# Kernel optimization log

Measured on AMD Instinct MI355X. Metric: run time of the kernel, lower is better.

The kernel has to match this reference:

```python
import jax, jax.numpy as jnp
import numpy as np

# MACE/molgym-style SimpleModel with max_ell=1, hidden_irreps = 64x0e + 64x1o,
# num_interactions=2, num_elements=10, num_bessel=8, polynomial cutoff p=5, r_max=5.0.
N, E, C, NE, NB, H = 20000, 320000, 64, 10, 8, 64
R_MAX = 5.0
P_CUT = 5


def _mlp(x, W1, W2, W3):
    # radial MLP producing per-edge tensor-product weights (silu nonlinearity)
    h = jax.nn.silu(x @ W1)
    h = jax.nn.silu(h @ W2)
    return h @ W3


def setup_inputs() -> dict:
    key = jax.random.key(0)
    ks = jax.random.split(key, 24)
    positions = jax.random.normal(ks[0], (N, 3), jnp.float32)
    edge_index = jax.random.randint(ks[1], (2, E), 0, N)
    shifts = jnp.zeros((E, 3), jnp.float32)
    species = jax.random.randint(ks[2], (N,), 0, NE)
    node_attrs = jax.nn.one_hot(species, NE, dtype=jnp.float32)

    def w(k, shape, fan_in):
        return jax.random.normal(k, shape, jnp.float32) / np.sqrt(fan_in)

    params = dict(
        W_embed=w(ks[3], (NE, C), NE),
        R1_W1=w(ks[4], (NB, H), NB), R1_W2=w(ks[5], (H, H), H), R1_W3=w(ks[6], (H, 2 * C), H),
        U1_s=w(ks[7], (C, C), C),
        L1_s=w(ks[8], (C, C), C), L1_v=w(ks[9], (C, C), C),
        K1_s=w(ks[10], (C, NE, C), C * NE),
        R2_W1=w(ks[11], (NB, H), NB), R2_W2=w(ks[12], (H, H), H), R2_W3=w(ks[13], (H, 4 * C), H),
        U2_s=w(ks[14], (C, C), C), U2_v=w(ks[15], (C, C), C),
        L2_s=w(ks[16], (2 * C, C), 2 * C), L2_v=w(ks[17], (2 * C, C), 2 * C),
        K2_s=w(ks[18], (C, NE, C), C * NE), K2_v=w(ks[19], (C, NE, C), C * NE),
    )
    return dict(positions=positions, node_attrs=node_attrs, edge_index=edge_index,
                shifts=shifts, **params)


def _forward(positions, node_attrs, shifts, W_embed,
             R1_W1, R1_W2, R1_W3, U1_s, L1_s, L1_v, K1_s,
             R2_W1, R2_W2, R2_W3, U2_s, U2_v, L2_s, L2_v, K2_s, K2_v,
             edge_index):
    snd, rcv = edge_index[0], edge_index[1]
    # edge vectors / lengths
    vec = positions[snd] - positions[rcv] + shifts            # [E,3]
    length = jnp.sqrt(jnp.sum(vec * vec, axis=1, keepdims=True) + 1e-12)  # [E,1]
    unit = vec / length
    # spherical harmonics (normalize=True, component normalization): Y0=1, Y1=sqrt(3)*r_hat
    Y1 = np.float32(np.sqrt(3.0)) * unit                      # [E,3]
    # Bessel radial basis * polynomial cutoff
    n = jnp.arange(1, NB + 1, dtype=jnp.float32)
    bessel = np.float32(np.sqrt(2.0 / R_MAX)) * jnp.sin(n * np.float32(np.pi) * length / R_MAX) / length
    u = length / R_MAX
    p = P_CUT
    poly = (1.0 - 0.5 * (p + 1) * (p + 2) * u ** p
            + p * (p + 2) * u ** (p + 1)
            - 0.5 * p * (p + 1) * u ** (p + 2))
    edge_feats = bessel * (poly * (u < 1.0))                  # [E,NB]
    # node embedding (linear on one-hot species)
    s0 = node_attrs @ W_embed                                 # [N,C]

    # ---- interaction block 1 (input feats: scalars only) ----
    s = s0 @ U1_s                                             # linear_up
    tpw = _mlp(edge_feats, R1_W1, R1_W2, R1_W3).reshape(E, 2, C)
    s_e = s[snd]                                              # gather sender feats
    m_s = tpw[:, 0] * s_e                                     # 0e x 0e -> 0e  [E,C]
    m_v = (tpw[:, 1] * s_e)[:, :, None] * Y1[:, None, :]      # 0e x 1o -> 1o  [E,C,3]
    agg_s = jax.ops.segment_sum(m_s, rcv, num_segments=N)
    agg_v = jax.ops.segment_sum(m_v, rcv, num_segments=N)
    skip_s = jnp.einsum('nu,nv,uvd->nd', s0, node_attrs, K1_s)  # skip tensor product
    s1 = agg_s @ L1_s + skip_s                                # [N,C]
    v1 = jnp.einsum('nci,cd->ndi', agg_v, L1_v)               # [N,C,3]

    # ---- interaction block 2 (input feats: 64x0e + 64x1o) ----
    s = s1 @ U2_s
    v = jnp.einsum('nci,cd->ndi', v1, U2_v)
    tpw = _mlp(edge_feats, R2_W1, R2_W2, R2_W3).reshape(E, 4, C)
    s_e, v_e = s[snd], v[snd]
    mA = tpw[:, 0] * s_e                                      # 0e x 0e -> 0e
    mB = (tpw[:, 1] * s_e)[:, :, None] * Y1[:, None, :]       # 0e x 1o -> 1o
    mC = tpw[:, 2][:, :, None] * v_e                          # 1o x 0e -> 1o
    mD = tpw[:, 3] * (jnp.einsum('eci,ei->ec', v_e, Y1) / np.float32(np.sqrt(3.0)))  # 1o x 1o -> 0e
    mid_s = jnp.concatenate([mA, mD], axis=1)                 # [E,2C]
    mid_v = jnp.concatenate([mB, mC], axis=1)                 # [E,2C,3]
    agg_s = jax.ops.segment_sum(mid_s, rcv, num_segments=N)
    agg_v = jax.ops.segment_sum(mid_v, rcv, num_segments=N)
    skip_s = jnp.einsum('nu,nv,uvd->nd', s1, node_attrs, K2_s)
    skip_v = jnp.einsum('nui,nv,uvd->ndi', v1, node_attrs, K2_v)
    s2 = agg_s @ L2_s + skip_s                                # [N,C]
    v2 = jnp.einsum('nci,cd->ndi', agg_v, L2_v) + skip_v      # [N,C,3]
    return jnp.concatenate([s2, v2.reshape(N, 3 * C)], axis=1)  # [N,4C]


def reference(positions, node_attrs, edge_index, shifts, W_embed,
              R1_W1, R1_W2, R1_W3, U1_s, L1_s, L1_v, K1_s,
              R2_W1, R2_W2, R2_W3, U2_s, U2_v, L2_s, L2_v, K2_s, K2_v):
    return _forward(positions, node_attrs, shifts, W_embed,
                    R1_W1, R1_W2, R1_W3, U1_s, L1_s, L1_v, K1_s,
                    R2_W1, R2_W2, R2_W3, U2_s, U2_v, L2_s, L2_v, K2_s, K2_v,
                    edge_index)
```

## Files before the change

kernel.cpp:

```cpp
#include <hip/hip_runtime.h>

#define NNODES 20000
#define NEDGES 320000
#define NELEM  10
#define NC     (NNODES * 64)

#define OFF_SUP1 ((size_t)0)
#define OFF_AGS1 ((size_t)1 * NC)
#define OFF_AGV1 ((size_t)2 * NC)
#define OFF_AGS2 ((size_t)0)
#define OFF_AGV2 ((size_t)2 * NC)
#define OFF_SUP2 ((size_t)8 * NC)
#define OFF_VUP2 ((size_t)9 * NC)
#define OFF_SKS2 ((size_t)12 * NC)
#define OFF_SKV2 ((size_t)13 * NC)
#define OFF_INT  ((size_t)16 * NC)

#define SMEM_BYTES 52480

typedef __attribute__((ext_vector_type(8))) short bf16x8;
typedef __attribute__((ext_vector_type(4))) float f32x4;

__device__ __forceinline__ float silu(float x) { return x / (1.0f + __expf(-x)); }
__device__ __forceinline__ int rfl(int v) { return __builtin_amdgcn_readfirstlane(v); }
__device__ __forceinline__ int rl_i(int v, int l) { return __builtin_amdgcn_readlane(v, l); }
__device__ __forceinline__ float rl_f(float v, int l) {
    return __int_as_float(__builtin_amdgcn_readlane(__float_as_int(v), l));
}
__device__ __forceinline__ uint2 split2(float x0, float x1) {
    unsigned int b0 = __float_as_uint(x0), b1 = __float_as_uint(x1);
    unsigned int h0 = (b0 + 0x7FFF + ((b0 >> 16) & 1)) & 0xFFFF0000u;
    unsigned int h1 = (b1 + 0x7FFF + ((b1 >> 16) & 1)) & 0xFFFF0000u;
    unsigned int l0 = __float_as_uint(x0 - __uint_as_float(h0));
    unsigned int l1 = __float_as_uint(x1 - __uint_as_float(h1));
    unsigned int hi = (h0 >> 16) | (h1 & 0xFFFF0000u);
    unsigned int lo = ((l0 + 0x7FFF + ((l0 >> 16) & 1)) >> 16)
                    | ((l1 + 0x7FFF + ((l1 >> 16) & 1)) & 0xFFFF0000u);
    return make_uint2(hi, lo);
}

__global__ __launch_bounds__(256) void k_wsplit(
    const float* __restrict__ W3a, const float* __restrict__ W3b,
    unsigned short* __restrict__ out)
{
    int t = blockIdx.x * 256 + threadIdx.x;
    float x; unsigned short *ph, *pl; int idx;
    if (t < 8192) {
        int n = t >> 6, k = t & 63;
        x = W3a[k * 128 + n]; ph = out; pl = out + 8192; idx = n * 64 + k;
    } else {
        int u = t - 8192; int n = u >> 6, k = u & 63;
        x = W3b[k * 256 + n]; ph = out + 16384; pl = out + 32768; idx = n * 64 + k;
    }
    unsigned int b = __float_as_uint(x);
    unsigned int h = (b + 0x7FFF + ((b >> 16) & 1)) & 0xFFFF0000u;
    unsigned int r = __float_as_uint(x - __uint_as_float(h));
    ph[idx] = (unsigned short)(h >> 16);
    pl[idx] = (unsigned short)((r + 0x7FFF + ((r >> 16) & 1)) >> 16);
}

__global__ __launch_bounds__(256) void k_hist(const int* __restrict__ eidx,
                                              int* __restrict__ hist)
{
    int e = blockIdx.x * 256 + threadIdx.x;
    atomicAdd(&hist[eidx[NEDGES + e]], 1);
}

__global__ __launch_bounds__(1024) void k_scan(const int* __restrict__ hist,
                                               int* __restrict__ cursor)
{
    __shared__ int wsum[16];
    __shared__ int gbase;
    int tid = threadIdx.x;
    int lane = tid & 63, wvid = tid >> 6;
    if (tid == 0) gbase = 0;
    __syncthreads();
    for (int seg = 0; seg < 20; ++seg) {
        int i = seg * 1024 + tid;
        int v = (i < NNODES) ? hist[i] : 0;
        int s = v;
        #pragma unroll
        for (int d = 1; d < 64; d <<= 1) {
            int t = __shfl_up(s, d, 64);
            if (lane >= d) s += t;
        }
        if (lane == 63) wsum[wvid] = s;
        __syncthreads();
        if (wvid == 0) {
            int w = (lane < 16) ? wsum[lane] : 0;
            #pragma unroll
            for (int d = 1; d < 16; d <<= 1) {
                int t = __shfl_up(w, d, 64);
                if (lane >= d) w += t;
            }
            if (lane < 16) wsum[lane] = w;
        }
        __syncthreads();
        int wbase = (wvid == 0) ? 0 : wsum[wvid - 1];
        if (i < NNODES) cursor[i] = gbase + wbase + s - v;
        int segtot = wsum[15];
        __syncthreads();
        if (tid == 0) gbase += segtot;
    }
}

__global__ __launch_bounds__(256) void k_scatter(const int* __restrict__ eidx,
                                                 int* __restrict__ cursor,
                                                 int* __restrict__ sorted)
{
    int e = blockIdx.x * 256 + threadIdx.x;
    int pos = atomicAdd(&cursor[eidx[NEDGES + e]], 1);
    sorted[pos] = e;
}

__global__ __launch_bounds__(256) void k_node_pre(
    const float* __restrict__ attrs, const float* __restrict__ Wemb,
    const float* __restrict__ U1s, float* __restrict__ sUp1)
{
    int lane = threadIdx.x & 63, wv = threadIdx.x >> 6;
    int n = blockIdx.x * 4 + wv;
    __shared__ __align__(16) float s0sh[4][64];
    float s0 = 0.f;
    #pragma unroll
    for (int v = 0; v < NELEM; ++v) s0 += attrs[n * NELEM + v] * Wemb[v * 64 + lane];
    s0sh[wv][lane] = s0;
    __syncthreads();
    float a = 0.f;
    #pragma unroll 8
    for (int k = 0; k < 64; ++k) a += s0sh[wv][k] * U1s[k * 64 + lane];
    sUp1[n * 64 + lane] = a;
}

__global__ __launch_bounds__(256, 3) void k_edge1(
    const float* __restrict__ pos, const int* __restrict__ eidx,
    const float* __restrict__ shf, const int* __restrict__ sorted,
    const float* __restrict__ W1, const float* __restrict__ W2,
    const unsigned short* __restrict__ w3h, const unsigned short* __restrict__ w3l,
    const float* __restrict__ sUp1,
    float* __restrict__ agS1, float* __restrict__ agV1)
{
    __shared__ __align__(16) char smem[SMEM_BYTES];
    float (*ysh)[3]   = (float (*)[3])(smem);
    int*  ssh         = (int*)(smem + 768);
    int*  rsh         = (int*)(smem + 1024);
    float (*h1sh)[65] = (float (*)[65])(smem + 1280);
    float (*fsh)[9]   = (float (*)[9])(smem + 17920);
    unsigned short (*h2buf)[64][72] = (unsigned short (*)[64][72])(smem + 34048);

    const int tid = threadIdx.x;
    const int lane = tid & 63;
    const int w = rfl(tid >> 6);
    const int e0 = blockIdx.x * 64;

    {
        int e = tid >> 2, sub = tid & 3;
        int sid = sorted[e0 + e];
        int snd = eidx[sid], rcv = eidx[NEDGES + sid];
        float dx = pos[snd * 3 + 0] - pos[rcv * 3 + 0] + shf[(size_t)sid * 3 + 0];
        float dy = pos[snd * 3 + 1] - pos[rcv * 3 + 1] + shf[(size_t)sid * 3 + 1];
        float dz = pos[snd * 3 + 2] - pos[rcv * 3 + 2] + shf[(size_t)sid * 3 + 2];
        float len = sqrtf(dx * dx + dy * dy + dz * dz + 1e-12f);
        float inv = 1.0f / len;
        float u = len * 0.2f;
        float u2 = u * u, u4 = u2 * u2, u5 = u4 * u, u6 = u5 * u, u7 = u6 * u;
        float cut = (u < 1.0f) ? (1.0f - 21.0f * u5 + 35.0f * u6 - 15.0f * u7) : 0.0f;
        float s = 0.632455532033676f * inv * cut;
        #pragma unroll
        for (int kk = 0; kk < 2; ++kk) {
            int k = sub * 2 + kk;
            fsh[e][k] = s * sinf((float)(k + 1) * 0.628318530717959f * len);
        }
        if (sub == 0) {
            ssh[e] = snd; rsh[e] = rcv;
            ysh[e][0] = 1.73205080756888f * dx * inv;
            ysh[e][1] = 1.73205080756888f * dy * inv;
            ysh[e][2] = 1.73205080756888f * dz * inv;
        }
    }
    __syncthreads();

    const int rAll = rsh[lane];
    const int sAll = ssh[lane];
    const float y0A = ysh[lane][0], y1A = ysh[lane][1], y2A = ysh[lane][2];

    {
        float f[8];
        #pragma unroll
        for (int k = 0; k < 8; ++k) f[k] = fsh[lane][k];
        const float* __restrict__ w1b = W1 + w * 16;
        #pragma unroll
        for (int j = 0; j < 16; ++j) {
            float a = 0.f;
            #pragma unroll
            for (int k = 0; k < 8; ++k) a = fmaf(f[k], w1b[k * 64 + j], a);
            h1sh[lane][w * 16 + j] = silu(a);
        }
    }
    __syncthreads();

    {
        const float2* __restrict__ w2b = (const float2*)W2 + w * 8;
        float2 acc[8];
        #pragma unroll
        for (int j = 0; j < 8; ++j) acc[j] = make_float2(0.f, 0.f);
        for (int k = 0; k < 64; ++k) {
            float h = h1sh[lane][k];
            const float2* __restrict__ wk = w2b + k * 32;
            #pragma unroll
            for (int j = 0; j < 8; ++j) {
                float2 wv = wk[j];
                acc[j].x = fmaf(h, wv.x, acc[j].x);
                acc[j].y = fmaf(h, wv.y, acc[j].y);
            }
        }
        #pragma unroll
        for (int j = 0; j < 8; ++j) {
            uint2 p = split2(silu(acc[j].x), silu(acc[j].y));
            *(unsigned int*)&h2buf[0][lane][w * 16 + 2 * j] = p.x;
            *(unsigned int*)&h2buf[1][lane][w * 16 + 2 * j] = p.y;
        }
    }
    __syncthreads();

    const int q = lane >> 4, nl = lane & 15;
    float* trw = (float*)(smem + 1280) + w * 2048;

    const unsigned short* ar = &h2buf[0][w * 16 + nl][0];
    const unsigned short* al = &h2buf[1][w * 16 + nl][0];
    bf16x8 ah0 = *(const bf16x8*)(ar + q * 8);
    bf16x8 ah1 = *(const bf16x8*)(ar + 32 + q * 8);
    bf16x8 al0 = *(const bf16x8*)(al + q * 8);
    bf16x8 al1 = *(const bf16x8*)(al + 32 + q * 8);

    float sreg[16];
    #pragma unroll
    for (int i = 0; i < 16; ++i)
        sreg[i] = sUp1[rl_i(sAll, w * 16 + i) * 64 + lane];

    #pragma unroll
    for (int nt = 0; nt < 8; ++nt) {
        int ng = nt * 16 + nl;
        const unsigned short* wh = w3h + ng * 64 + q * 8;
        const unsigned short* wl = w3l + ng * 64 + q * 8;
        bf16x8 bh0 = *(const bf16x8*)wh;
        bf16x8 bh1 = *(const bf16x8*)(wh + 32);
        bf16x8 bl0 = *(const bf16x8*)wl;
        bf16x8 bl1 = *(const bf16x8*)(wl + 32);
        f32x4 a = {0.f, 0.f, 0.f, 0.f};
        a = __builtin_amdgcn_mfma_f32_16x16x32_bf16(ah0, bh0, a, 0, 0, 0);
        a = __builtin_amdgcn_mfma_f32_16x16x32_bf16(ah1, bh1, a, 0, 0, 0);
        a = __builtin_amdgcn_mfma_f32_16x16x32_bf16(ah0, bl0, a, 0, 0, 0);
        a = __builtin_amdgcn_mfma_f32_16x16x32_bf16(ah1, bl1, a, 0, 0, 0);
        a = __builtin_amdgcn_mfma_f32_16x16x32_bf16(al0, bh0, a, 0, 0, 0);
        a = __builtin_amdgcn_mfma_f32_16x16x32_bf16(al1, bh1, a, 0, 0, 0);
        #pragma unroll
        for (int r = 0; r < 4; ++r) {
            int li = q * 4 + r;
            trw[li * 128 + ((ng + 4 * li) & 127)] = a[r];
        }
    }

    float accS = 0.f, b0 = 0.f, b1 = 0.f, b2 = 0.f;
    int cur = rl_i(rAll, w * 16);
    #pragma unroll
    for (int i = 0; i < 16; ++i) {
        int e = w * 16 + i;
        int rcv = rl_i(rAll, e);
        if (rcv != cur) {
            unsafeAtomicAdd(&agS1[cur * 64 + lane], accS);
            unsafeAtomicAdd(&agV1[cur * 192 +       lane], b0);
            unsafeAtomicAdd(&agV1[cur * 192 +  64 + lane], b1);
            unsafeAtomicAdd(&agV1[cur * 192 + 128 + lane], b2);
            accS = b0 = b1 = b2 = 0.f;
            cur = rcv;
        }
        float tv0 = trw[i * 128 + ((lane + 4 * i) & 127)];
        float tv1 = trw[i * 128 + ((64 + lane + 4 * i) & 127)];
        float se = sreg[i];
        accS += tv0 * se;
        float msg = tv1 * se;
        b0 += msg * rl_f(y0A, e);
        b1 += msg * rl_f(y1A, e);
        b2 += msg * rl_f(y2A, e);
    }
    unsafeAtomicAdd(&agS1[cur * 64 + lane], accS);
    unsafeAtomicAdd(&agV1[cur * 192 +       lane], b0);
    unsafeAtomicAdd(&agV1[cur * 192 +  64 + lane], b1);
    unsafeAtomicAdd(&agV1[cur * 192 + 128 + lane], b2);
}

__global__ __launch_bounds__(256) void k_node_mid(
    const float* __restrict__ attrs, const float* __restrict__ Wemb,
    const float* __restrict__ K1s, const float* __restrict__ L1s,
    const float* __restrict__ L1v,
    const float* __restrict__ U2s, const float* __restrict__ U2v,
    const float* __restrict__ K2s, const float* __restrict__ K2v,
    const float* __restrict__ agS1, const float* __restrict__ agV1,
    float* __restrict__ sUp2, float* __restrict__ vUp2,
    float* __restrict__ skS2, float* __restrict__ skV2)
{
    int lane = threadIdx.x & 63, wv = threadIdx.x >> 6;
    int n = blockIdx.x * 4 + wv;
    __shared__ float aSsh[4][64];
    __shared__ float aVsh[4][3][64];
    __shared__ float s0sh[4][64];
    __shared__ float s1sh[4][64];
    __shared__ float v1sh[4][3][64];

    int sp = 0;
    #pragma unroll
    for (int v = 0; v < NELEM; ++v) if (attrs[n * NELEM + v] > 0.5f) sp = v;
    aSsh[wv][lane] = agS1[n * 64 + lane];
    #pragma unroll
    for (int i = 0; i < 3; ++i) aVsh[wv][i][lane] = agV1[n * 192 + i * 64 + lane];
    s0sh[wv][lane] = Wemb[sp * 64 + lane];
    __syncthreads();

    float s1 = 0.f;
    #pragma unroll 8
    for (int k = 0; k < 64; ++k) s1 += aSsh[wv][k] * L1s[k * 64 + lane];
    #pragma unroll 8
    for (int k = 0; k < 64; ++k) s1 += s0sh[wv][k] * K1s[(k * NELEM + sp) * 64 + lane];
    float v1[3] = {0.f, 0.f, 0.f};
    #pragma unroll 8
    for (int k = 0; k < 64; ++k) {
        float w = L1v[k * 64 + lane];
        v1[0] += aVsh[wv][0][k] * w;
        v1[1] += aVsh[wv][1][k] * w;
        v1[2] += aVsh[wv][2][k] * w;
    }
    s1sh[wv][lane] = s1;
    #pragma unroll
    for (int i = 0; i < 3; ++i) v1sh[wv][i][lane] = v1[i];
    __syncthreads();

    float su = 0.f, ks = 0.f;
    float vu[3] = {0.f, 0.f, 0.f}, kv[3] = {0.f, 0.f, 0.f};
    #pragma unroll 8
    for (int k = 0; k < 64; ++k) su += s1sh[wv][k] * U2s[k * 64 + lane];
    #pragma unroll 8
    for (int k = 0; k < 64; ++k) ks += s1sh[wv][k] * K2s[(k * NELEM + sp) * 64 + lane];
    #pragma unroll 8
    for (int k = 0; k < 64; ++k) {
        float w = U2v[k * 64 + lane];
        vu[0] += v1sh[wv][0][k] * w;
        vu[1] += v1sh[wv][1][k] * w;
        vu[2] += v1sh[wv][2][k] * w;
    }
    #pragma unroll 8
    for (int k = 0; k < 64; ++k) {
        float w = K2v[(k * NELEM + sp) * 64 + lane];
        kv[0] += v1sh[wv][0][k] * w;
        kv[1] += v1sh[wv][1][k] * w;
        kv[2] += v1sh[wv][2][k] * w;
    }
    sUp2[n * 64 + lane] = su;
    skS2[n * 64 + lane] = ks;
    #pragma unroll
    for (int i = 0; i < 3; ++i) {
        vUp2[n * 192 + i * 64 + lane] = vu[i];
        skV2[n * 192 + i * 64 + lane] = kv[i];
    }
}

__global__ __launch_bounds__(256, 3) void k_edge2(
    const float* __restrict__ pos, const int* __restrict__ eidx,
    const float* __restrict__ shf, const int* __restrict__ sorted,
    const float* __restrict__ W1, const float* __restrict__ W2,
    const unsigned short* __restrict__ w3h, const unsigned short* __restrict__ w3l,
    const float* __restrict__ sUp2, const float* __restrict__ vUp2,
    float* __restrict__ agS2, float* __restrict__ agV2)
{
    __shared__ __align__(16) char smem[SMEM_BYTES];
    float (*ysh)[3]   = (float (*)[3])(smem);
    int*  ssh         = (int*)(smem + 768);
    int*  rsh         = (int*)(smem + 1024);
    float (*h1sh)[65] = (float (*)[65])(smem + 1280);
    float (*fsh)[9]   = (float (*)[9])(smem + 17920);
    unsigned short (*h2buf)[64][72] = (unsigned short (*)[64][72])(smem + 34048);

    const int tid = threadIdx.x;
    const int lane = tid & 63;
    const int w = rfl(tid >> 6);
    const int e0 = blockIdx.x * 64;

    {
        int e = tid >> 2, sub = tid & 3;
        int sid = sorted[e0 + e];
        int snd = eidx[sid], rcv = eidx[NEDGES + sid];
        float dx = pos[snd * 3 + 0] - pos[rcv * 3 + 0] + shf[(size_t)sid * 3 + 0];
        float dy = pos[snd * 3 + 1] - pos[rcv * 3 + 1] + shf[(size_t)sid * 3 + 1];
        float dz = pos[snd * 3 + 2] - pos[rcv * 3 + 2] + shf[(size_t)sid * 3 + 2];
        float len = sqrtf(dx * dx + dy * dy + dz * dz + 1e-12f);
        float inv = 1.0f / len;
        float u = len * 0.2f;
        float u2 = u * u, u4 = u2 * u2, u5 = u4 * u, u6 = u5 * u, u7 = u6 * u;
        float cut = (u < 1.0f) ? (1.0f - 21.0f * u5 + 35.0f * u6 - 15.0f * u7) : 0.0f;
        float s = 0.632455532033676f * inv * cut;
        #pragma unroll
        for (int kk = 0; kk < 2; ++kk) {
            int k = sub * 2 + kk;
            fsh[e][k] = s * sinf((float)(k + 1) * 0.628318530717959f * len);
        }
        if (sub == 0) {
            ssh[e] = snd; rsh[e] = rcv;
            ysh[e][0] = 1.73205080756888f * dx * inv;
            ysh[e][1] = 1.73205080756888f * dy * inv;
            ysh[e][2] = 1.73205080756888f * dz * inv;
        }
    }
    __syncthreads();

    const int rAll = rsh[lane];
    const int sAll = ssh[lane];
    const float y0A = ysh[lane][0], y1A = ysh[lane][1], y2A = ysh[lane][2];

    {
        float f[8];
        #pragma unroll
        for (int k = 0; k < 8; ++k) f[k] = fsh[lane][k];
        const float* __restrict__ w1b = W1 + w * 16;
        #pragma unroll
        for (int j = 0; j < 16; ++j) {
            float a = 0.f;
            #pragma unroll
            for (int k = 0; k < 8; ++k) a = fmaf(f[k], w1b[k * 64 + j], a);
            h1sh[lane][w * 16 + j] = silu(a);
        }
    }
    __syncthreads();

    {
        const float2* __restrict__ w2b = (const float2*)W2 + w * 8;
        float2 acc[8];
        #pragma unroll
        for (int j = 0; j < 8; ++j) acc[j] = make_float2(0.f, 0.f);
        for (int k = 0; k < 64; ++k) {
            float h = h1sh[lane][k];
            const float2* __restrict__ wk = w2b + k * 32;
            #pragma unroll
            for (int j = 0; j < 8; ++j) {
                float2 wv = wk[j];
                acc[j].x = fmaf(h, wv.x, acc[j].x);
                acc[j].y = fmaf(h, wv.y, acc[j].y);
            }
        }
        #pragma unroll
        for (int j = 0; j < 8; ++j) {
            uint2 p = split2(silu(acc[j].x), silu(acc[j].y));
            *(unsigned int*)&h2buf[0][lane][w * 16 + 2 * j] = p.x;
            *(unsigned int*)&h2buf[1][lane][w * 16 + 2 * j] = p.y;
        }
    }
    __syncthreads();

    const int q = lane >> 4, nl = lane & 15;
    float* trw = (float*)(smem + 1280) + w * 2048;

    const unsigned short* ar = &h2buf[0][w * 16 + nl][0];
    const unsigned short* al = &h2buf[1][w * 16 + nl][0];
    bf16x8 ah0 = *(const bf16x8*)(ar + q * 8);
    bf16x8 ah1 = *(const bf16x8*)(ar + 32 + q * 8);
    bf16x8 al0 = *(const bf16x8*)(al + q * 8);
    bf16x8 al1 = *(const bf16x8*)(al + 32 + q * 8);

    float sreg[16];
    #pragma unroll
    for (int i = 0; i < 16; ++i)
        sreg[i] = sUp2[rl_i(sAll, w * 16 + i) * 64 + lane];

    #pragma unroll
    for (int nt = 0; nt < 8; ++nt) {
        int ng = nt * 16 + nl;
        const unsigned short* wh = w3h + ng * 64 + q * 8;
        const unsigned short* wl = w3l + ng * 64 + q * 8;
        bf16x8 bh0 = *(const bf16x8*)wh;
        bf16x8 bh1 = *(const bf16x8*)(wh + 32);
        bf16x8 bl0 = *(const bf16x8*)wl;
        bf16x8 bl1 = *(const bf16x8*)(wl + 32);
        f32x4 a = {0.f, 0.f, 0.f, 0.f};
        a = __builtin_amdgcn_mfma_f32_16x16x32_bf16(ah0, bh0, a, 0, 0, 0);
        a = __builtin_amdgcn_mfma_f32_16x16x32_bf16(ah1, bh1, a, 0, 0, 0);
        a = __builtin_amdgcn_mfma_f32_16x16x32_bf16(ah0, bl0, a, 0, 0, 0);
        a = __builtin_amdgcn_mfma_f32_16x16x32_bf16(ah1, bl1, a, 0, 0, 0);
        a = __builtin_amdgcn_mfma_f32_16x16x32_bf16(al0, bh0, a, 0, 0, 0);
        a = __builtin_amdgcn_mfma_f32_16x16x32_bf16(al1, bh1, a, 0, 0, 0);
        #pragma unroll
        for (int r = 0; r < 4; ++r) {
            int li = q * 4 + r;
            trw[li * 128 + ((ng + 4 * li) & 127)] = a[r];
        }
    }

    {
        float accS = 0.f, b0 = 0.f, b1 = 0.f, b2 = 0.f;
        int cur = rl_i(rAll, w * 16);
        #pragma unroll
        for (int i = 0; i < 16; ++i) {
            int e = w * 16 + i;
            int rcv = rl_i(rAll, e);
            if (rcv != cur) {
                unsafeAtomicAdd(&agS2[cur * 128 + lane], accS);
                unsafeAtomicAdd(&agV2[cur * 384 + 0 * 128 + lane], b0);
                unsafeAtomicAdd(&agV2[cur * 384 + 1 * 128 + lane], b1);
                unsafeAtomicAdd(&agV2[cur * 384 + 2 * 128 + lane], b2);
                accS = b0 = b1 = b2 = 0.f;
                cur = rcv;
            }
            float tv0 = trw[i * 128 + ((lane + 4 * i) & 127)];
            float tv1 = trw[i * 128 + ((64 + lane + 4 * i) & 127)];
            float se = sreg[i];
            accS += tv0 * se;
            float msg = tv1 * se;
            b0 += msg * rl_f(y0A, e);
            b1 += msg * rl_f(y1A, e);
            b2 += msg * rl_f(y2A, e);
        }
        unsafeAtomicAdd(&agS2[cur * 128 + lane], accS);
        unsafeAtomicAdd(&agV2[cur * 384 + 0 * 128 + lane], b0);
        unsafeAtomicAdd(&agV2[cur * 384 + 1 * 128 + lane], b1);
        unsafeAtomicAdd(&agV2[cur * 384 + 2 * 128 + lane], b2);
    }

    float vr0[16], vr1[16], vr2[16];
    #pragma unroll
    for (int i = 0; i < 16; ++i) {
        int snd = rl_i(sAll, w * 16 + i);
        vr0[i] = vUp2[snd * 192 +       lane];
        vr1[i] = vUp2[snd * 192 +  64 + lane];
        vr2[i] = vUp2[snd * 192 + 128 + lane];
    }

    #pragma unroll
    for (int nt = 0; nt < 8; ++nt) {
        int c  = nt * 16 + nl;
        int ng = 128 + c;
        const unsigned short* wh = w3h + ng * 64 + q * 8;
        const unsigned short* wl = w3l + ng * 64 + q * 8;
        bf16x8 bh0 = *(const bf16x8*)wh;
        bf16x8 bh1 = *(const bf16x8*)(wh + 32);
        bf16x8 bl0 = *(const bf16x8*)wl;
        bf16x8 bl1 = *(const bf16x8*)(wl + 32);
        f32x4 a = {0.f, 0.f, 0.f, 0.f};
        a = __builtin_amdgcn_mfma_f32_16x16x32_bf16(ah0, bh0, a, 0, 0, 0);
        a = __builtin_amdgcn_mfma_f32_16x16x32_bf16(ah1, bh1, a, 0, 0, 0);
        a = __builtin_amdgcn_mfma_f32_16x16x32_bf16(ah0, bl0, a, 0, 0, 0);
        a = __builtin_amdgcn_mfma_f32_16x16x32_bf16(ah1, bl1, a, 0, 0, 0);
        a = __builtin_amdgcn_mfma_f32_16x16x32_bf16(al0, bh0, a, 0, 0, 0);
        a = __builtin_amdgcn_mfma_f32_16x16x32_bf16(al1, bh1, a, 0, 0, 0);
        #pragma unroll
        for (int r = 0; r < 4; ++r) {
            int li = q * 4 + r;
            trw[li * 128 + ((c + 4 * li) & 127)] = a[r];
        }
    }

    {
        float accD = 0.f, c0 = 0.f, c1 = 0.f, c2 = 0.f;
        int cur = rl_i(rAll, w * 16);
        #pragma unroll
        for (int i = 0; i < 16; ++i) {
            int e = w * 16 + i;
            int rcv = rl_i(rAll, e);
            if (rcv != cur) {
                unsafeAtomicAdd(&agS2[cur * 128 + 64 + lane], accD);
                unsafeAtomicAdd(&agV2[cur * 384 + 0 * 128 + 64 + lane], c0);
                unsafeAtomicAdd(&agV2[cur * 384 + 1 * 128 + 64 + lane], c1);
                unsafeAtomicAdd(&agV2[cur * 384 + 2 * 128 + 64 + lane], c2);
                accD = c0 = c1 = c2 = 0.f;
                cur = rcv;
            }
            float tvC = trw[i * 128 + ((lane + 4 * i) & 127)];
            float tvD = trw[i * 128 + ((64 + lane + 4 * i) & 127)];
            c0 += tvC * vr0[i];
            c1 += tvC * vr1[i];
            c2 += tvC * vr2[i];
            float dotvy = vr0[i] * rl_f(y0A, e) + vr1[i] * rl_f(y1A, e)
                        + vr2[i] * rl_f(y2A, e);
            accD += tvD * dotvy * 0.577350269189626f;
        }
        unsafeAtomicAdd(&agS2[cur * 128 + 64 + lane], accD);
        unsafeAtomicAdd(&agV2[cur * 384 + 0 * 128 + 64 + lane], c0);
        unsafeAtomicAdd(&agV2[cur * 384 + 1 * 128 + 64 + lane], c1);
        unsafeAtomicAdd(&agV2[cur * 384 + 2 * 128 + 64 + lane], c2);
    }
}

__global__ __launch_bounds__(256) void k_node_out(
    const float* __restrict__ L2s, const float* __restrict__ L2v,
    const float* __restrict__ agS2, const float* __restrict__ agV2,
    const float* __restrict__ skS2, const float* __restrict__ skV2,
    float* __restrict__ out)
{
    int lane = threadIdx.x & 63, wv = threadIdx.x >> 6;
    int n = blockIdx.x * 4 + wv;
    __shared__ __align__(16) float aS[4][128];
    __shared__ __align__(16) float aV[4][3][128];

    aS[wv][lane]      = agS2[n * 128 + lane];
    aS[wv][64 + lane] = agS2[n * 128 + 64 + lane];
    #pragma unroll
    for (int i = 0; i < 3; ++i) {
        aV[wv][i][lane]      = agV2[n * 384 + i * 128 + lane];
        aV[wv][i][64 + lane] = agV2[n * 384 + i * 128 + 64 + lane];
    }
    __syncthreads();

    float s2 = skS2[n * 64 + lane];
    #pragma unroll 8
    for (int u = 0; u < 128; ++u) s2 += aS[wv][u] * L2s[u * 64 + lane];
    float v2[3];
    #pragma unroll
    for (int i = 0; i < 3; ++i) v2[i] = skV2[n * 192 + i * 64 + lane];
    #pragma unroll 8
    for (int u = 0; u < 128; ++u) {
        float w = L2v[u * 64 + lane];
        v2[0] += aV[wv][0][u] * w;
        v2[1] += aV[wv][1][u] * w;
        v2[2] += aV[wv][2][u] * w;
    }
    out[(size_t)n * 256 + lane] = s2;
    #pragma unroll
    for (int i = 0; i < 3; ++i)
        out[(size_t)n * 256 + 64 + lane * 3 + i] = v2[i];
}

extern "C" void kernel_launch(void* const* d_in, const int* in_sizes, int n_in,
                              void* d_out, int out_size, void* d_ws, size_t ws_size,
                              hipStream_t stream)
{
    (void)in_sizes; (void)n_in; (void)out_size; (void)ws_size;
    const float* positions  = (const float*)d_in[0];
    const float* node_attrs = (const float*)d_in[1];
    const int*   edge_index = (const int*)d_in[2];
    const float* shifts     = (const float*)d_in[3];
    const float* W_embed    = (const float*)d_in[4];
    const float* R1W1 = (const float*)d_in[5];
    const float* R1W2 = (const float*)d_in[6];
    const float* R1W3 = (const float*)d_in[7];
    const float* U1s  = (const float*)d_in[8];
    const float* L1s  = (const float*)d_in[9];
    const float* L1v  = (const float*)d_in[10];
    const float* K1s  = (const float*)d_in[11];
    const float* R2W1 = (const float*)d_in[12];
    const float* R2W2 = (const float*)d_in[13];
    const float* R2W3 = (const float*)d_in[14];
    const float* U2s  = (const float*)d_in[15];
    const float* U2v  = (const float*)d_in[16];
    const float* L2s  = (const float*)d_in[17];
    const float* L2v  = (const float*)d_in[18];
    const float* K2s  = (const float*)d_in[19];
    const float* K2v  = (const float*)d_in[20];

    float* wsf = (float*)d_ws;
    int*   wsi = (int*)(wsf + OFF_INT);
    int* hist   = wsi;
    int* cursor = wsi + 20000;
    int* sorted = wsi + 40000;
    unsigned short* wsh = (unsigned short*)(wsi + 360000);
    const unsigned short* w3a_hi = wsh;
    const unsigned short* w3a_lo = wsh + 8192;
    const unsigned short* w3b_hi = wsh + 16384;
    const unsigned short* w3b_lo = wsh + 32768;

    hipMemsetAsync(wsf + OFF_AGS1, 0, (size_t)4 * NC * sizeof(float), stream);
    hipMemsetAsync(hist, 0, 20000 * sizeof(int), stream);

    k_wsplit<<<96, 256, 0, stream>>>(R1W3, R2W3, wsh);
    k_hist<<<NEDGES / 256, 256, 0, stream>>>(edge_index, hist);
    k_scan<<<1, 1024, 0, stream>>>(hist, cursor);
    k_scatter<<<NEDGES / 256, 256, 0, stream>>>(edge_index, cursor, sorted);

    k_node_pre<<<NNODES / 4, 256, 0, stream>>>(node_attrs, W_embed, U1s, wsf + OFF_SUP1);
    k_edge1<<<NEDGES / 64, 256, 0, stream>>>(positions, edge_index, shifts, sorted,
                                             R1W1, R1W2, w3a_hi, w3a_lo,
                                             wsf + OFF_SUP1, wsf + OFF_AGS1, wsf + OFF_AGV1);
    k_node_mid<<<NNODES / 4, 256, 0, stream>>>(node_attrs, W_embed, K1s, L1s, L1v,
                                               U2s, U2v, K2s, K2v,
                                               wsf + OFF_AGS1, wsf + OFF_AGV1,
                                               wsf + OFF_SUP2, wsf + OFF_VUP2,
                                               wsf + OFF_SKS2, wsf + OFF_SKV2);
    hipMemsetAsync(wsf + OFF_AGS2, 0, (size_t)8 * NC * sizeof(float), stream);
    k_edge2<<<NEDGES / 64, 256, 0, stream>>>(positions, edge_index, shifts, sorted,
                                             R2W1, R2W2, w3b_hi, w3b_lo,
                                             wsf + OFF_SUP2, wsf + OFF_VUP2,
                                             wsf + OFF_AGS2, wsf + OFF_AGV2);
    k_node_out<<<NNODES / 4, 256, 0, stream>>>(L2s, L2v, wsf + OFF_AGS2, wsf + OFF_AGV2,
                                               wsf + OFF_SKS2, wsf + OFF_SKV2,
                                               (float*)d_out);
}
```

Measured before the change: 633.1 us.

## Halve per-wave tpw staging buffer to shrink LDS and raise edge-kernel occupancy

```diff
diff --git a/kernel.cpp b/kernel.cpp
--- a/kernel.cpp
+++ b/kernel.cpp
@@ -16,7 +16,7 @@
 #define OFF_SKV2 ((size_t)13 * NC)
 #define OFF_INT  ((size_t)16 * NC)
 
-#define SMEM_BYTES 52480
+#define SMEM_BYTES 38656
 
 typedef __attribute__((ext_vector_type(8))) short bf16x8;
 typedef __attribute__((ext_vector_type(4))) float f32x4;
@@ -131,7 +131,7 @@
     sUp1[n * 64 + lane] = a;
 }
 
-__global__ __launch_bounds__(256, 3) void k_edge1(
+__global__ __launch_bounds__(256, 4) void k_edge1(
     const float* __restrict__ pos, const int* __restrict__ eidx,
     const float* __restrict__ shf, const int* __restrict__ sorted,
     const float* __restrict__ W1, const float* __restrict__ W2,
@@ -144,8 +144,8 @@
     int*  ssh         = (int*)(smem + 768);
     int*  rsh         = (int*)(smem + 1024);
     float (*h1sh)[65] = (float (*)[65])(smem + 1280);
-    float (*fsh)[9]   = (float (*)[9])(smem + 17920);
-    unsigned short (*h2buf)[64][72] = (unsigned short (*)[64][72])(smem + 34048);
+    unsigned short (*h2buf)[64][72] = (unsigned short (*)[64][72])(smem + 17920);
+    float (*fsh)[9]   = (float (*)[9])(smem + 36352);
 
     const int tid = threadIdx.x;
     const int lane = tid & 63;
@@ -223,7 +223,7 @@
     __syncthreads();
 
     const int q = lane >> 4, nl = lane & 15;
-    float* trw = (float*)(smem + 1280) + w * 2048;
+    float* trw = (float*)(smem + 1280) + w * 1024;
 
     const unsigned short* ar = &h2buf[0][w * 16 + nl][0];
     const unsigned short* al = &h2buf[1][w * 16 + nl][0];
@@ -238,8 +238,47 @@
         sreg[i] = sUp1[rl_i(sAll, w * 16 + i) * 64 + lane];
 
     #pragma unroll
-    for (int nt = 0; nt < 8; ++nt) {
-        int ng = nt * 16 + nl;
+    for (int nt = 0; nt < 4; ++nt) {
+        int c = nt * 16 + nl;
+        const unsigned short* wh = w3h + c * 64 + q * 8;
+        const unsigned short* wl = w3l + c * 64 + q * 8;
+        bf16x8 bh0 = *(const bf16x8*)wh;
+        bf16x8 bh1 = *(const bf16x8*)(wh + 32);
+        bf16x8 bl0 = *(const bf16x8*)wl;
+        bf16x8 bl1 = *(const bf16x8*)(wl + 32);
+        f32x4 a = {0.f, 0.f, 0.f, 0.f};
+        a = __builtin_amdgcn_mfma_f32_16x16x32_bf16(ah0, bh0, a, 0, 0, 0);
+        a = __builtin_amdgcn_mfma_f32_16x16x32_bf16(ah1, bh1, a, 0, 0, 0);
+        a = __builtin_amdgcn_mfma_f32_16x16x32_bf16(ah0, bl0, a, 0, 0, 0);
+        a = __builtin_amdgcn_mfma_f32_16x16x32_bf16(ah1, bl1, a, 0, 0, 0);
+        a = __builtin_amdgcn_mfma_f32_16x16x32_bf16(al0, bh0, a, 0, 0, 0);
+        a = __builtin_amdgcn_mfma_f32_16x16x32_bf16(al1, bh1, a, 0, 0, 0);
+        #pragma unroll
+        for (int r = 0; r < 4; ++r) {
+            int li = q * 4 + r;
+            trw[li * 64 + ((c + 4 * li) & 63)] = a[r];
+        }
+    }
+    {
+        float accS = 0.f;
+        int cur = rl_i(rAll, w * 16);
+        #pragma unroll
+        for (int i = 0; i < 16; ++i) {
+            int e = w * 16 + i;
+            int rcv = rl_i(rAll, e);
+            if (rcv != cur) {
+                unsafeAtomicAdd(&agS1[cur * 64 + lane], accS);
+                accS = 0.f; cur = rcv;
+            }
+            accS += trw[i * 64 + ((lane + 4 * i) & 63)] * sreg[i];
+        }
+        unsafeAtomicAdd(&agS1[cur * 64 + lane], accS);
+    }
+
+    #pragma unroll
+    for (int nt = 0; nt < 4; ++nt) {
+        int c = nt * 16 + nl;
+        int ng = 64 + c;
         const unsigned short* wh = w3h + ng * 64 + q * 8;
         const unsigned short* wl = w3l + ng * 64 + q * 8;
         bf16x8 bh0 = *(const bf16x8*)wh;
@@ -256,37 +295,31 @@
         #pragma unroll
         for (int r = 0; r < 4; ++r) {
             int li = q * 4 + r;
-            trw[li * 128 + ((ng + 4 * li) & 127)] = a[r];
-        }
-    }
-
-    float accS = 0.f, b0 = 0.f, b1 = 0.f, b2 = 0.f;
-    int cur = rl_i(rAll, w * 16);
-    #pragma unroll
-    for (int i = 0; i < 16; ++i) {
-        int e = w * 16 + i;
-        int rcv = rl_i(rAll, e);
-        if (rcv != cur) {
-            unsafeAtomicAdd(&agS1[cur * 64 + lane], accS);
-            unsafeAtomicAdd(&agV1[cur * 192 +       lane], b0);
-            unsafeAtomicAdd(&agV1[cur * 192 +  64 + lane], b1);
-            unsafeAtomicAdd(&agV1[cur * 192 + 128 + lane], b2);
-            accS = b0 = b1 = b2 = 0.f;
-            cur = rcv;
-        }
-        float tv0 = trw[i * 128 + ((lane + 4 * i) & 127)];
-        float tv1 = trw[i * 128 + ((64 + lane + 4 * i) & 127)];
-        float se = sreg[i];
-        accS += tv0 * se;
-        float msg = tv1 * se;
-        b0 += msg * rl_f(y0A, e);
-        b1 += msg * rl_f(y1A, e);
-        b2 += msg * rl_f(y2A, e);
-    }
-    unsafeAtomicAdd(&agS1[cur * 64 + lane], accS);
-    unsafeAtomicAdd(&agV1[cur * 192 +       lane], b0);
-    unsafeAtomicAdd(&agV1[cur * 192 +  64 + lane], b1);
-    unsafeAtomicAdd(&agV1[cur * 192 + 128 + lane], b2);
+            trw[li * 64 + ((c + 4 * li) & 63)] = a[r];
+        }
+    }
+    {
+        float b0 = 0.f, b1 = 0.f, b2 = 0.f;
+        int cur = rl_i(rAll, w * 16);
+        #pragma unroll
+        for (int i = 0; i < 16; ++i) {
+            int e = w * 16 + i;
+            int rcv = rl_i(rAll, e);
+            if (rcv != cur) {
+                unsafeAtomicAdd(&agV1[cur * 192 +       lane], b0);
+                unsafeAtomicAdd(&agV1[cur * 192 +  64 + lane], b1);
+                unsafeAtomicAdd(&agV1[cur * 192 + 128 + lane], b2);
+                b0 = b1 = b2 = 0.f; cur = rcv;
+            }
+            float msg = trw[i * 64 + ((lane + 4 * i) & 63)] * sreg[i];
+            b0 += msg * rl_f(y0A, e);
+            b1 += msg * rl_f(y1A, e);
+            b2 += msg * rl_f(y2A, e);
+        }
+        unsafeAtomicAdd(&agV1[cur * 192 +       lane], b0);
+        unsafeAtomicAdd(&agV1[cur * 192 +  64 + lane], b1);
+        unsafeAtomicAdd(&agV1[cur * 192 + 128 + lane], b2);
+    }
 }
 
 __global__ __launch_bounds__(256) void k_node_mid(
@@ -363,7 +396,7 @@
     }
 }
 
-__global__ __launch_bounds__(256, 3) void k_edge2(
+__global__ __launch_bounds__(256, 4) void k_edge2(
     const float* __restrict__ pos, const int* __restrict__ eidx,
     const float* __restrict__ shf, const int* __restrict__ sorted,
     const float* __restrict__ W1, const float* __restrict__ W2,
@@ -376,8 +409,8 @@
     int*  ssh         = (int*)(smem + 768);
     int*  rsh         = (int*)(smem + 1024);
     float (*h1sh)[65] = (float (*)[65])(smem + 1280);
-    float (*fsh)[9]   = (float (*)[9])(smem + 17920);
-    unsigned short (*h2buf)[64][72] = (unsigned short (*)[64][72])(smem + 34048);
+    unsigned short (*h2buf)[64][72] = (unsigned short (*)[64][72])(smem + 17920);
+    float (*fsh)[9]   = (float (*)[9])(smem + 36352);
 
     const int tid = threadIdx.x;
     const int lane = tid & 63;
@@ -455,7 +488,7 @@
     __syncthreads();
 
     const int q = lane >> 4, nl = lane & 15;
-    float* trw = (float*)(smem + 1280) + w * 2048;
+    float* trw = (float*)(smem + 1280) + w * 1024;
 
     const unsigned short* ar = &h2buf[0][w * 16 + nl][0];
     const unsigned short* al = &h2buf[1][w * 16 + nl][0];
@@ -470,8 +503,47 @@
         sreg[i] = sUp2[rl_i(sAll, w * 16 + i) * 64 + lane];
 
     #pragma unroll
-    for (int nt = 0; nt < 8; ++nt) {
-        int ng = nt * 16 + nl;
+    for (int nt = 0; nt < 4; ++nt) {
+        int c = nt * 16 + nl;
+        const unsigned short* wh = w3h + c * 64 + q * 8;
+        const unsigned short* wl = w3l + c * 64 + q * 8;
+        bf16x8 bh0 = *(const bf16x8*)wh;
+        bf16x8 bh1 = *(const bf16x8*)(wh + 32);
+        bf16x8 bl0 = *(const bf16x8*)wl;
+        bf16x8 bl1 = *(const bf16x8*)(wl + 32);
+        f32x4 a = {0.f, 0.f, 0.f, 0.f};
+        a = __builtin_amdgcn_mfma_f32_16x16x32_bf16(ah0, bh0, a, 0, 0, 0);
+        a = __builtin_amdgcn_mfma_f32_16x16x32_bf16(ah1, bh1, a, 0, 0, 0);
+        a = __builtin_amdgcn_mfma_f32_16x16x32_bf16(ah0, bl0, a, 0, 0, 0);
+        a = __builtin_amdgcn_mfma_f32_16x16x32_bf16(ah1, bl1, a, 0, 0, 0);
+        a = __builtin_amdgcn_mfma_f32_16x16x32_bf16(al0, bh0, a, 0, 0, 0);
+        a = __builtin_amdgcn_mfma_f32_16x16x32_bf16(al1, bh1, a, 0, 0, 0);
+        #pragma unroll
+        for (int r = 0; r < 4; ++r) {
+            int li = q * 4 + r;
+            trw[li * 64 + ((c + 4 * li) & 63)] = a[r];
+        }
+    }
+    {
+        float accS = 0.f;
+        int cur = rl_i(rAll, w * 16);
+        #pragma unroll
+        for (int i = 0; i < 16; ++i) {
+            int e = w * 16 + i;
+            int rcv = rl_i(rAll, e);
+            if (rcv != cur) {
+                unsafeAtomicAdd(&agS2[cur * 128 + lane], accS);
+                accS = 0.f; cur = rcv;
+            }
+            accS += trw[i * 64 + ((lane + 4 * i) & 63)] * sreg[i];
+        }
+        unsafeAtomicAdd(&agS2[cur * 128 + lane], accS);
+    }
+
+    #pragma unroll
+    for (int nt = 0; nt < 4; ++nt) {
+        int c = nt * 16 + nl;
+        int ng = 64 + c;
         const unsigned short* wh = w3h + ng * 64 + q * 8;
         const unsigned short* wl = w3l + ng * 64 + q * 8;
         bf16x8 bh0 = *(const bf16x8*)wh;
@@ -488,35 +560,27 @@
         #pragma unroll
         for (int r = 0; r < 4; ++r) {
             int li = q * 4 + r;
-            trw[li * 128 + ((ng + 4 * li) & 127)] = a[r];
-        }
-    }
-
-    {
-        float accS = 0.f, b0 = 0.f, b1 = 0.f, b2 = 0.f;
+            trw[li * 64 + ((c + 4 * li) & 63)] = a[r];
+        }
+    }
+    {
+        float b0 = 0.f, b1 = 0.f, b2 = 0.f;
         int cur = rl_i(rAll, w * 16);
         #pragma unroll
         for (int i = 0; i < 16; ++i) {
             int e = w * 16 + i;
             int rcv = rl_i(rAll, e);
             if (rcv != cur) {
-                unsafeAtomicAdd(&agS2[cur * 128 + lane], accS);
                 unsafeAtomicAdd(&agV2[cur * 384 + 0 * 128 + lane], b0);
                 unsafeAtomicAdd(&agV2[cur * 384 + 1 * 128 + lane], b1);
                 unsafeAtomicAdd(&agV2[cur * 384 + 2 * 128 + lane], b2);
-                accS = b0 = b1 = b2 = 0.f;
-                cur = rcv;
-            }
-            float tv0 = trw[i * 128 + ((lane + 4 * i) & 127)];
-            float tv1 = trw[i * 128 + ((64 + lane + 4 * i) & 127)];
-            float se = sreg[i];
-            accS += tv0 * se;
-            float msg = tv1 * se;
+                b0 = b1 = b2 = 0.f; cur = rcv;
+            }
+            float msg = trw[i * 64 + ((lane + 4 * i) & 63)] * sreg[i];
             b0 += msg * rl_f(y0A, e);
             b1 += msg * rl_f(y1A, e);
             b2 += msg * rl_f(y2A, e);
         }
-        unsafeAtomicAdd(&agS2[cur * 128 + lane], accS);
         unsafeAtomicAdd(&agV2[cur * 384 + 0 * 128 + lane], b0);
         unsafeAtomicAdd(&agV2[cur * 384 + 1 * 128 + lane], b1);
         unsafeAtomicAdd(&agV2[cur * 384 + 2 * 128 + lane], b2);
@@ -532,8 +596,8 @@
     }
 
     #pragma unroll
-    for (int nt = 0; nt < 8; ++nt) {
-        int c  = nt * 16 + nl;
+    for (int nt = 0; nt < 4; ++nt) {
+        int c = nt * 16 + nl;
         int ng = 128 + c;
         const unsigned short* wh = w3h + ng * 64 + q * 8;
         const unsigned short* wl = w3l + ng * 64 + q * 8;
@@ -551,12 +615,57 @@
         #pragma unroll
         for (int r = 0; r < 4; ++r) {
             int li = q * 4 + r;
-            trw[li * 128 + ((c + 4 * li) & 127)] = a[r];
-        }
-    }
-
-    {
-        float accD = 0.f, c0 = 0.f, c1 = 0.f, c2 = 0.f;
+            trw[li * 64 + ((c + 4 * li) & 63)] = a[r];
+        }
+    }
+    {
+        float c0 = 0.f, c1 = 0.f, c2 = 0.f;
+        int cur = rl_i(rAll, w * 16);
+        #pragma unroll
+        for (int i = 0; i < 16; ++i) {
+            int e = w * 16 + i;
+            int rcv = rl_i(rAll, e);
+            if (rcv != cur) {
+                unsafeAtomicAdd(&agV2[cur * 384 + 0 * 128 + 64 + lane], c0);
+                unsafeAtomicAdd(&agV2[cur * 384 + 1 * 128 + 64 + lane], c1);
+                unsafeAtomicAdd(&agV2[cur * 384 + 2 * 128 + 64 + lane], c2);
+                c0 = c1 = c2 = 0.f; cur = rcv;
+            }
+            float tvC = trw[i * 64 + ((lane + 4 * i) & 63)];
+            c0 += tvC * vr0[i];
+            c1 += tvC * vr1[i];
+            c2 += tvC * vr2[i];
+        }
+        unsafeAtomicAdd(&agV2[cur * 384 + 0 * 128 + 64 + lane], c0);
+        unsafeAtomicAdd(&agV2[cur * 384 + 1 * 128 + 64 + lane], c1);
+        unsafeAtomicAdd(&agV2[cur * 384 + 2 * 128 + 64 + lane], c2);
+    }
+
+    #pragma unroll
+    for (int nt = 0; nt < 4; ++nt) {
+        int c = nt * 16 + nl;
+        int ng = 192 + c;
+        const unsigned short* wh = w3h + ng * 64 + q * 8;
+        const unsigned short* wl = w3l + ng * 64 + q * 8;
+        bf16x8 bh0 = *(const bf16x8*)wh;
+        bf16x8 bh1 = *(const bf16x8*)(wh + 32);
+        bf16x8 bl0 = *(const bf16x8*)wl;
+        bf16x8 bl1 = *(const bf16x8*)(wl + 32);
+        f32x4 a = {0.f, 0.f, 0.f, 0.f};
+        a = __builtin_amdgcn_mfma_f32_16x16x32_bf16(ah0, bh0, a, 0, 0, 0);
+        a = __builtin_amdgcn_mfma_f32_16x16x32_bf16(ah1, bh1, a, 0, 0, 0);
+        a = __builtin_amdgcn_mfma_f32_16x16x32_bf16(ah0, bl0, a, 0, 0, 0);
+        a = __builtin_amdgcn_mfma_f32_16x16x32_bf16(ah1, bl1, a, 0, 0, 0);
+        a = __builtin_amdgcn_mfma_f32_16x16x32_bf16(al0, bh0, a, 0, 0, 0);
+        a = __builtin_amdgcn_mfma_f32_16x16x32_bf16(al1, bh1, a, 0, 0, 0);
+        #pragma unroll
+        for (int r = 0; r < 4; ++r) {
+            int li = q * 4 + r;
+            trw[li * 64 + ((c + 4 * li) & 63)] = a[r];
+        }
+    }
+    {
+        float accD = 0.f;
         int cur = rl_i(rAll, w * 16);
         #pragma unroll
         for (int i = 0; i < 16; ++i) {
@@ -564,25 +673,14 @@
             int rcv = rl_i(rAll, e);
             if (rcv != cur) {
                 unsafeAtomicAdd(&agS2[cur * 128 + 64 + lane], accD);
-                unsafeAtomicAdd(&agV2[cur * 384 + 0 * 128 + 64 + lane], c0);
-                unsafeAtomicAdd(&agV2[cur * 384 + 1 * 128 + 64 + lane], c1);
-                unsafeAtomicAdd(&agV2[cur * 384 + 2 * 128 + 64 + lane], c2);
-                accD = c0 = c1 = c2 = 0.f;
-                cur = rcv;
-            }
-            float tvC = trw[i * 128 + ((lane + 4 * i) & 127)];
-            float tvD = trw[i * 128 + ((64 + lane + 4 * i) & 127)];
-            c0 += tvC * vr0[i];
-            c1 += tvC * vr1[i];
-            c2 += tvC * vr2[i];
+                accD = 0.f; cur = rcv;
+            }
+            float tvD = trw[i * 64 + ((lane + 4 * i) & 63)];
             float dotvy = vr0[i] * rl_f(y0A, e) + vr1[i] * rl_f(y1A, e)
                         + vr2[i] * rl_f(y2A, e);
             accD += tvD * dotvy * 0.577350269189626f;
         }
         unsafeAtomicAdd(&agS2[cur * 128 + 64 + lane], accD);
-        unsafeAtomicAdd(&agV2[cur * 384 + 0 * 128 + 64 + lane], c0);
-        unsafeAtomicAdd(&agV2[cur * 384 + 1 * 128 + 64 + lane], c1);
-        unsafeAtomicAdd(&agV2[cur * 384 + 2 * 128 + 64 + lane], c2);
     }
 }
 
```

Result: slower. 648.3 us (+2.4%).
